# Kernel tuning notes

Measured on AMD Instinct MI355X. Metric: run time of the kernel, lower is better.

The kernel has to match this reference:

```python
import jax, jax.numpy as jnp
import numpy as np

N_NODES = 50000
NEG_SLOPE = 0.2  # PyG GATConv default
EPS = 1e-16      # PyG softmax denominator epsilon


def _gat_conv(x, edge_index, W, att_src, att_dst, bias):
    """Single-head PyG-style GATConv with self-loops.
    x: [N, F_in], edge_index: [2, E] (row 0 = src/j, row 1 = dst/i).
    """
    n = x.shape[0]
    loop = jnp.arange(n, dtype=edge_index.dtype)
    src = jnp.concatenate([edge_index[0], loop])  # [E+N]
    dst = jnp.concatenate([edge_index[1], loop])  # [E+N]

    h = x @ W                                      # [N, F_out]
    a_src = h @ att_src                            # [N]
    a_dst = h @ att_dst                            # [N]

    e = jax.nn.leaky_relu(a_src[src] + a_dst[dst], NEG_SLOPE)  # [E+N]
    # segment softmax over incoming edges of each dst node
    m = jax.ops.segment_max(e, dst, num_segments=n)
    m = jnp.where(jnp.isfinite(m), m, 0.0)
    e = jnp.exp(e - m[dst])
    s = jax.ops.segment_sum(e, dst, num_segments=n)
    alpha = e / (s[dst] + EPS)                     # [E+N]

    out = jax.ops.segment_sum(alpha[:, None] * h[src], dst, num_segments=n)
    return out + bias


def setup_inputs() -> dict:
    key = jax.random.key(0)
    ks = jax.random.split(key, 10)
    d_in, d_hid, d_emb = 128, 64, 64
    n_edges = 800000
    x = jax.random.normal(ks[0], (N_NODES, d_in), dtype=jnp.float32)
    edge_index = jax.random.randint(ks[1], (2, n_edges), 0, N_NODES, dtype=jnp.int64)
    def glorot(k, shape):
        lim = float(np.sqrt(6.0 / sum(shape)))
        return jax.random.uniform(k, shape, jnp.float32, -lim, lim)
    return {
        "x": x,
        "edge_index": edge_index,
        "W1": glorot(ks[2], (d_in, d_hid)),
        "att_src1": glorot(ks[3], (d_hid,)),
        "att_dst1": glorot(ks[4], (d_hid,)),
        "b1": jnp.zeros((d_hid,), jnp.float32),
        "W2": glorot(ks[5], (d_hid, d_emb)),
        "att_src2": glorot(ks[6], (d_emb,)),
        "att_dst2": glorot(ks[7], (d_emb,)),
        "b2": jnp.zeros((d_emb,), jnp.float32),
    }


def reference(x, edge_index, W1, att_src1, att_dst1, b1, W2, att_src2, att_dst2, b2):
    x1 = jax.nn.relu(_gat_conv(x, edge_index, W1, att_src1, att_dst1, b1))
    # dropout is identity in eval mode
    x2 = _gat_conv(x1, edge_index, W2, att_src2, att_dst2, b2)
    return x2
```

## Files before the change

kernel.cpp:

```cpp
#include <hip/hip_runtime.h>
#include <hip/hip_bf16.h>

#define F_OUT 64
#define NEG_SLOPE 0.2f
#define SOFT_EPS 1e-16f
#define BW 256
#define CH 8192
#define TH 512

typedef short short8 __attribute__((ext_vector_type(8)));
typedef float floatx4 __attribute__((ext_vector_type(4)));
typedef unsigned short ushort4v __attribute__((ext_vector_type(4)));

__device__ __forceinline__ unsigned short f2bf_bits(float v) {
    __hip_bfloat16 hb = __float2bfloat16(v);
    return *(unsigned short*)&hb;
}
__device__ __forceinline__ float bf_bits2f(unsigned short u) {
    __hip_bfloat16 hb = *(__hip_bfloat16*)&u;
    return __bfloat162float(hb);
}
__device__ __forceinline__ float read_any(const void* src, int off, int bf) {
    return bf ? __bfloat162float(((const __hip_bfloat16*)src)[off])
              : ((const float*)src)[off];
}
__device__ __forceinline__ int get_idx(const void* ei, int i64, long long pos) {
    return i64 ? (int)((const long long*)ei)[pos] : ((const int*)ei)[pos];
}

__device__ __forceinline__ void detect_local(const unsigned* wbits, const unsigned* ebits,
                                             int* sm_bf, int* sm_i64) {
    if (threadIdx.x < 64) {
        unsigned w = wbits[threadIdx.x];
        unsigned e = (w >> 7) & 0xFFu;
        unsigned long long mb = __ballot(e >= 0x60u && e <= 0x7Eu);
        unsigned long long mz = __ballot(ebits[2 * threadIdx.x + 1] == 0u);
        if (threadIdx.x == 0) { *sm_bf = (__popcll(mb) > 32); *sm_i64 = (__popcll(mz) > 32); }
    }
    __syncthreads();
}

__global__ void count_prep(const void* __restrict__ ei, int* __restrict__ table,
                           const void* w1, const void* as1, const void* ad1, const void* b1,
                           const void* w2, const void* as2, const void* ad2, const void* b2,
                           unsigned short* __restrict__ wt1, unsigned short* __restrict__ wt2,
                           float* __restrict__ vecs, int* __restrict__ flags,
                           int E, int total, int NB, int nchunks, int n1, int n2, int K1) {
    __shared__ int cnt[1024];
    __shared__ int s_bf, s_i64;
    detect_local((const unsigned*)w1, (const unsigned*)ei, &s_bf, &s_i64);
    int bf = s_bf, i64 = s_i64;
    int g = blockIdx.x, tid = threadIdx.x;
    if (g == 0 && tid == 0) { flags[0] = bf; flags[1] = i64; }

    if (g < nchunks) {
        for (int k = tid; k < NB; k += TH) cnt[k] = 0;
        __syncthreads();
        int base = g * CH;
        int lim = base + CH < total ? base + CH : total;
        for (int t = base + tid; t < lim; t += TH) {
            int i = t < E ? get_idx(ei, i64, (long long)E + t) : t - E;
            atomicAdd(&cnt[i >> 8], 1);
        }
        __syncthreads();
        for (int k = tid; k < NB; k += TH) table[k * nchunks + g] = cnt[k];
    } else {
        int wtotal = n1 + n2 + 384;
        for (int t = tid; t < wtotal; t += TH) {
            if (t < n1) {
                int n = t / K1, k = t - n * K1;
                wt1[t] = f2bf_bits(read_any(w1, k * F_OUT + n, bf));
            } else if (t < n1 + n2) {
                int u = t - n1;
                int n = u >> 6, k = u & 63;
                wt2[u] = f2bf_bits(read_any(w2, k * F_OUT + n, bf));
            } else {
                int u = t - n1 - n2;
                const void* srcp[6] = {as1, ad1, b1, as2, ad2, b2};
                vecs[u] = read_any(srcp[u >> 6], u & 63, bf);
            }
        }
    }
}

template <int K, int WAVES>
__device__ __forceinline__ void gemm_body(int blk, int tid,
                          const void* __restrict__ xv, const unsigned short* __restrict__ Wt,
                          const float* __restrict__ att_s, const float* __restrict__ att_d,
                          unsigned short* __restrict__ h, float* __restrict__ a_s,
                          float* __restrict__ a_d, int N, int bf) {
    int lane = tid & 63;
    int m0 = (blk * WAVES + (tid >> 6)) * 16;
    if (m0 >= N) return;
    int c = lane & 15, quad = lane >> 4;
    int arow = m0 + c;
    if (arow >= N) arow = N - 1;

    floatx4 acc0 = {0.f, 0.f, 0.f, 0.f};
    floatx4 acc1 = acc0, acc2 = acc0, acc3 = acc0;

    for (int kc = 0; kc < K; kc += 32) {
        int ka = kc + quad * 8;
        short8 a;
        if (bf) {
            a = *(const short8*)((const unsigned short*)xv + (size_t)arow * K + ka);
        } else {
            const float* xp = (const float*)xv + (size_t)arow * K + ka;
#pragma unroll
            for (int j = 0; j < 8; ++j) a[j] = (short)f2bf_bits(xp[j]);
        }
        short8 b0 = *(const short8*)(Wt + (size_t)(c)      * K + ka);
        short8 b1 = *(const short8*)(Wt + (size_t)(16 + c) * K + ka);
        short8 b2 = *(const short8*)(Wt + (size_t)(32 + c) * K + ka);
        short8 b3 = *(const short8*)(Wt + (size_t)(48 + c) * K + ka);
        acc0 = __builtin_amdgcn_mfma_f32_16x16x32_bf16(a, b0, acc0, 0, 0, 0);
        acc1 = __builtin_amdgcn_mfma_f32_16x16x32_bf16(a, b1, acc1, 0, 0, 0);
        acc2 = __builtin_amdgcn_mfma_f32_16x16x32_bf16(a, b2, acc2, 0, 0, 0);
        acc3 = __builtin_amdgcn_mfma_f32_16x16x32_bf16(a, b3, acc3, 0, 0, 0);
    }

    float as0 = att_s[c],      as1 = att_s[16 + c], as2 = att_s[32 + c], as3 = att_s[48 + c];
    float ad0 = att_d[c],      ad1 = att_d[16 + c], ad2 = att_d[32 + c], ad3 = att_d[48 + c];
#pragma unroll
    for (int reg = 0; reg < 4; ++reg) {
        int row = m0 + quad * 4 + reg;
        float vs = acc0[reg] * as0 + acc1[reg] * as1 + acc2[reg] * as2 + acc3[reg] * as3;
        float vd = acc0[reg] * ad0 + acc1[reg] * ad1 + acc2[reg] * ad2 + acc3[reg] * ad3;
#pragma unroll
        for (int off = 1; off < 16; off <<= 1) {
            vs += __shfl_xor(vs, off);
            vd += __shfl_xor(vd, off);
        }
        if (row < N) {
            if (c == 0) { a_s[row] = vs; a_d[row] = vd; }
            unsigned short* hr = h + (size_t)row * F_OUT + c;
            hr[0]  = f2bf_bits(acc0[reg]);
            hr[16] = f2bf_bits(acc1[reg]);
            hr[32] = f2bf_bits(acc2[reg]);
            hr[48] = f2bf_bits(acc3[reg]);
        }
    }
}

__global__ void __launch_bounds__(TH)
scatter_gemm1(const void* __restrict__ ei, const int* __restrict__ table,
              unsigned* __restrict__ staged, int* __restrict__ segbeg,
              int* __restrict__ row_ptr, const void* __restrict__ xv,
              const unsigned short* __restrict__ Wt,
              const float* __restrict__ att_s, const float* __restrict__ att_d,
              unsigned short* __restrict__ h, float* __restrict__ a_s,
              float* __restrict__ a_d, const unsigned* __restrict__ wbits,
              int E, int total, int NB, int nchunks, int N) {
    __shared__ int s_bf, s_i64;
    detect_local(wbits, (const unsigned*)ei, &s_bf, &s_i64);
    int tid = threadIdx.x;
    if ((int)blockIdx.x >= nchunks) {
        gemm_body<128, 8>(blockIdx.x - nchunks, tid, xv, Wt, att_s, att_d,
                          h, a_s, a_d, N, s_bf);
        return;
    }
    __shared__ int s_scan[TH];
    __shared__ int s_cur[1024];
    int g = blockIdx.x;
    int i64 = s_i64;
    int b0 = 0;
    if (tid < NB) {
        const int* row = table + (size_t)tid * nchunks;
        int rsum = 0, rpart = 0;
        for (int c2 = 0; c2 < nchunks; ++c2) {
            int v = row[c2];
            rsum += v;
            rpart += (c2 < g) ? v : 0;
        }
        b0 = rsum;
        s_cur[tid] = rpart;
    }
    s_scan[tid] = (tid < NB) ? b0 : 0;
    __syncthreads();
    for (int off = 1; off < TH; off <<= 1) {
        int v = (tid >= off) ? s_scan[tid - off] : 0;
        __syncthreads();
        s_scan[tid] += v;
        __syncthreads();
    }
    if (tid < NB) {
        int excl = s_scan[tid] - b0;
        s_cur[tid] = excl + s_cur[tid];
        if (g == 0) segbeg[tid] = excl;
    }
    if (g == 0 && tid == 0) { segbeg[NB] = total; row_ptr[N] = total; }
    __syncthreads();
    int base = g * CH;
    int lim = base + CH < total ? base + CH : total;
    for (int t = base + tid; t < lim; t += TH) {
        int i = t < E ? get_idx(ei, i64, (long long)E + t) : t - E;
        int j = t < E ? get_idx(ei, i64, t) : t - E;
        int pos = atomicAdd(&s_cur[i >> 8], 1);
        staged[pos] = ((unsigned)(i & 255) << 24) | (unsigned)j;
    }
}

__global__ void bucket_csr(const unsigned* __restrict__ staged, const int* __restrict__ segbeg,
                           int* __restrict__ row_ptr, int* __restrict__ eidx, int N) {
    __shared__ int ldeg[BW];
    __shared__ int lcur[BW];
    __shared__ int wtot[4];
    int b = blockIdx.x;
    int t = threadIdx.x;
    int seg_beg = segbeg[b];
    int seg_end = segbeg[b + 1];
    ldeg[t] = 0;
    __syncthreads();
    for (int p = seg_beg + t; p < seg_end; p += 256)
        atomicAdd(&ldeg[staged[p] >> 24], 1);
    __syncthreads();
    int lane = t & 63, w = t >> 6;
    int d = ldeg[t];
    int v = d;
#pragma unroll
    for (int off = 1; off < 64; off <<= 1) {
        int u = __shfl_up(v, off);
        if (lane >= off) v += u;
    }
    if (lane == 63) wtot[w] = v;
    __syncthreads();
    int woff = 0;
    for (int k = 0; k < w; ++k) woff += wtot[k];
    int excl = v - d + woff;
    int node = b * BW + t;
    if (node < N) row_ptr[node] = seg_beg + excl;
    lcur[t] = excl;
    __syncthreads();
    for (int p = seg_beg + t; p < seg_end; p += 256) {
        unsigned pk = staged[p];
        int pos = atomicAdd(&lcur[pk >> 24], 1);
        eidx[seg_beg + pos] = (int)(pk & 0xFFFFFFu);
    }
}

__global__ void mfma_gemm2(const void* __restrict__ xv, const unsigned short* __restrict__ Wt,
                           const float* __restrict__ att_s, const float* __restrict__ att_d,
                           unsigned short* __restrict__ h, float* __restrict__ a_s,
                           float* __restrict__ a_d, int N) {
    gemm_body<64, 4>(blockIdx.x, threadIdx.x, xv, Wt, att_s, att_d, h, a_s, a_d, N, 1);
}

__global__ void node_gather(const int* __restrict__ row_ptr, const int* __restrict__ eidx,
                            const float* __restrict__ a_s, const float* __restrict__ a_d,
                            const unsigned short* __restrict__ h, const float* __restrict__ bias,
                            void* __restrict__ out, int N,
                            const int* __restrict__ flags, int mode) {
    int lane = threadIdx.x & 63;
    int i = blockIdx.x * 4 + (threadIdx.x >> 6);
    if (i >= N) return;
    int quad = lane >> 4, c = lane & 15;
    int beg = row_ptr[i];
    int end = row_ptr[i + 1];
    float ad = a_d[i];
    float se = 0.f;
    floatx4 acc[4];
#pragma unroll
    for (int k = 0; k < 4; ++k) acc[k] = (floatx4){0.f, 0.f, 0.f, 0.f};

    for (int p = beg; p < end; p += 64) {
        int tile = end - p; if (tile > 64) tile = 64;
        int jm = eidx[p + (lane < tile ? lane : tile - 1)];
        float wm = 0.f;
        if (lane < tile) {
            float e = a_s[jm] + ad;
            wm = __expf(e > 0.f ? e : NEG_SLOPE * e);
        }
        se += wm;
        for (int e = 0; e < tile; e += 16) {
#pragma unroll
            for (int k = 0; k < 4; ++k) {
                if (e + 4 * k < tile) {
                    int idx = e + 4 * k + quad;
                    int srcl = idx < tile ? idx : tile - 1;
                    int jk = __shfl(jm, srcl);
                    float wk = __shfl(wm, srcl);
                    if (idx >= tile) wk = 0.f;
                    ushort4v hv = *(const ushort4v*)(h + (size_t)jk * F_OUT + (c << 2));
                    acc[k][0] += wk * bf_bits2f(hv[0]);
                    acc[k][1] += wk * bf_bits2f(hv[1]);
                    acc[k][2] += wk * bf_bits2f(hv[2]);
                    acc[k][3] += wk * bf_bits2f(hv[3]);
                }
            }
        }
    }
#pragma unroll
    for (int off = 1; off < 64; off <<= 1) se += __shfl_xor(se, off);
    floatx4 A = (acc[0] + acc[1]) + (acc[2] + acc[3]);
#pragma unroll
    for (int m = 0; m < 4; ++m) {
        A[m] += __shfl_xor(A[m], 16);
        A[m] += __shfl_xor(A[m], 32);
    }
    if (quad == 0) {
        int col = c << 2;
        float inv = 1.f / (se + SOFT_EPS);
        float v0 = A[0] * inv + bias[col];
        float v1 = A[1] * inv + bias[col + 1];
        float v2 = A[2] * inv + bias[col + 2];
        float v3 = A[3] * inv + bias[col + 3];
        size_t o = (size_t)i * F_OUT + col;
        if (mode == 0) {
            ushort4v ov;
            ov[0] = f2bf_bits(v0 > 0.f ? v0 : 0.f);
            ov[1] = f2bf_bits(v1 > 0.f ? v1 : 0.f);
            ov[2] = f2bf_bits(v2 > 0.f ? v2 : 0.f);
            ov[3] = f2bf_bits(v3 > 0.f ? v3 : 0.f);
            *(ushort4v*)((unsigned short*)out + o) = ov;
        } else if (flags[0]) {
            ushort4v ov;
            ov[0] = f2bf_bits(v0); ov[1] = f2bf_bits(v1);
            ov[2] = f2bf_bits(v2); ov[3] = f2bf_bits(v3);
            *(ushort4v*)((unsigned short*)out + o) = ov;
        } else {
            floatx4 ov = {v0, v1, v2, v3};
            *(floatx4*)((float*)out + o) = ov;
        }
    }
}

extern "C" void kernel_launch(void* const* d_in, const int* in_sizes, int n_in,
                              void* d_out, int out_size, void* d_ws, size_t ws_size,
                              hipStream_t stream) {
    const void* x   = d_in[0];
    const void* ei  = d_in[1];
    const void* W1  = d_in[2];
    const void* as1 = d_in[3];
    const void* ad1 = d_in[4];
    const void* b1  = d_in[5];
    const void* W2  = d_in[6];
    const void* as2 = d_in[7];
    const void* ad2 = d_in[8];
    const void* b2  = d_in[9];

    int E  = in_sizes[1] / 2;
    int n1 = in_sizes[2];
    int n2 = in_sizes[6];
    int K1 = n1 / F_OUT;
    int N  = in_sizes[0] / K1;
    int total = E + N;
    int NB = (N + BW - 1) / BW;
    int nchunks = (total + CH - 1) / CH;
    int M = NB * nchunks;

    size_t nf = (size_t)N * F_OUT;
    char* wsb = (char*)d_ws;
    unsigned short* h   = (unsigned short*)wsb;
    unsigned short* x1b = h + nf;
    unsigned short* wt1 = x1b + nf;
    unsigned short* wt2 = wt1 + n1;
    float* a_s  = (float*)(wt2 + n2 + ((n1 + n2) & 1));
    float* a_d  = a_s + N;
    float* vecs = a_d + N;
    float* cAs1 = vecs,       *cAd1 = vecs + 64,  *cB1 = vecs + 128;
    float* cAs2 = vecs + 192, *cAd2 = vecs + 256, *cB2 = vecs + 320;
    int* flags    = (int*)(vecs + 384);
    int* row_ptr  = flags + 8;
    int* eidx     = row_ptr + N + 1;
    unsigned* staged = (unsigned*)(eidx + total);
    int* table    = (int*)(staged + total);
    int* segbeg   = table + M;

    int blkG1 = (N + 127) / 128;
    int blkG2 = (N + 63) / 64;
    int blkNode = (N + 3) / 4;

    count_prep<<<nchunks + 1, TH, 0, stream>>>(ei, table, W1, as1, ad1, b1,
                                               W2, as2, ad2, b2, wt1, wt2, vecs, flags,
                                               E, total, NB, nchunks, n1, n2, K1);
    scatter_gemm1<<<nchunks + blkG1, TH, 0, stream>>>(ei, table, staged, segbeg, row_ptr,
                                                      x, wt1, cAs1, cAd1, h, a_s, a_d,
                                                      (const unsigned*)W1,
                                                      E, total, NB, nchunks, N);
    bucket_csr<<<NB, 256, 0, stream>>>(staged, segbeg, row_ptr, eidx, N);
    node_gather<<<blkNode, 256, 0, stream>>>(row_ptr, eidx, a_s, a_d, h, cB1, x1b, N, flags, 0);
    mfma_gemm2<<<blkG2, 256, 0, stream>>>(x1b, wt2, cAs2, cAd2, h, a_s, a_d, N);
    node_gather<<<blkNode, 256, 0, stream>>>(row_ptr, eidx, a_s, a_d, h, cB2, d_out, N, flags, 1);
}
```

Before: 207.1 us.

## Fuse layer-1 gather with layer-2 GEMM in one kernel

```diff
diff --git a/kernel.cpp b/kernel.cpp
--- a/kernel.cpp
+++ b/kernel.cpp
@@ -238,22 +238,13 @@
     }
 }
 
-__global__ void mfma_gemm2(const void* __restrict__ xv, const unsigned short* __restrict__ Wt,
-                           const float* __restrict__ att_s, const float* __restrict__ att_d,
-                           unsigned short* __restrict__ h, float* __restrict__ a_s,
-                           float* __restrict__ a_d, int N) {
-    gemm_body<64, 4>(blockIdx.x, threadIdx.x, xv, Wt, att_s, att_d, h, a_s, a_d, N, 1);
-}
-
-__global__ void node_gather(const int* __restrict__ row_ptr, const int* __restrict__ eidx,
-                            const float* __restrict__ a_s, const float* __restrict__ a_d,
-                            const unsigned short* __restrict__ h, const float* __restrict__ bias,
-                            void* __restrict__ out, int N,
-                            const int* __restrict__ flags, int mode) {
-    int lane = threadIdx.x & 63;
-    int i = blockIdx.x * 4 + (threadIdx.x >> 6);
-    if (i >= N) return;
-    int quad = lane >> 4, c = lane & 15;
+__device__ __forceinline__ void gather_node(int i, int lane, int quad, int c,
+                                            const int* __restrict__ row_ptr,
+                                            const int* __restrict__ eidx,
+                                            const float* __restrict__ a_s,
+                                            const float* __restrict__ a_d,
+                                            const unsigned short* __restrict__ h,
+                                            float* se_out, floatx4* A_out) {
     int beg = row_ptr[i];
     int end = row_ptr[i + 1];
     float ad = a_d[i];
@@ -297,6 +288,99 @@
         A[m] += __shfl_xor(A[m], 16);
         A[m] += __shfl_xor(A[m], 32);
     }
+    *se_out = se;
+    *A_out = A;
+}
+
+#define XST 72
+__global__ void __launch_bounds__(1024)
+gather1_gemm2(const int* __restrict__ row_ptr, const int* __restrict__ eidx,
+              const float* __restrict__ a_s, const float* __restrict__ a_d,
+              const unsigned short* __restrict__ h, const float* __restrict__ bias,
+              const unsigned short* __restrict__ Wt2,
+              const float* __restrict__ att_s2, const float* __restrict__ att_d2,
+              unsigned short* __restrict__ h2, float* __restrict__ a_s2,
+              float* __restrict__ a_d2, int N) {
+    __shared__ unsigned short x1t[16 * XST];
+    int tid = threadIdx.x;
+    int lane = tid & 63;
+    int wv = tid >> 6;
+    int quad = lane >> 4, c = lane & 15;
+    int i = blockIdx.x * 16 + wv;
+
+    if (i < N) {
+        float se; floatx4 A;
+        gather_node(i, lane, quad, c, row_ptr, eidx, a_s, a_d, h, &se, &A);
+        if (quad == 0) {
+            int col = c << 2;
+            float inv = 1.f / (se + SOFT_EPS);
+            float v0 = A[0] * inv + bias[col];
+            float v1 = A[1] * inv + bias[col + 1];
+            float v2 = A[2] * inv + bias[col + 2];
+            float v3 = A[3] * inv + bias[col + 3];
+            ushort4v ov;
+            ov[0] = f2bf_bits(v0 > 0.f ? v0 : 0.f);
+            ov[1] = f2bf_bits(v1 > 0.f ? v1 : 0.f);
+            ov[2] = f2bf_bits(v2 > 0.f ? v2 : 0.f);
+            ov[3] = f2bf_bits(v3 > 0.f ? v3 : 0.f);
+            *(ushort4v*)(x1t + wv * XST + col) = ov;
+        }
+    } else if (quad == 0) {
+        *(ushort4v*)(x1t + wv * XST + (c << 2)) = (ushort4v){0, 0, 0, 0};
+    }
+    __syncthreads();
+
+    if (wv == 0) {
+        int m0 = blockIdx.x * 16;
+        floatx4 acc0 = {0.f, 0.f, 0.f, 0.f};
+        floatx4 acc1 = acc0, acc2 = acc0, acc3 = acc0;
+#pragma unroll
+        for (int kc = 0; kc < 64; kc += 32) {
+            int ka = kc + quad * 8;
+            short8 a = *(const short8*)(x1t + c * XST + ka);
+            short8 b0 = *(const short8*)(Wt2 + (size_t)(c)      * 64 + ka);
+            short8 b1 = *(const short8*)(Wt2 + (size_t)(16 + c) * 64 + ka);
+            short8 b2 = *(const short8*)(Wt2 + (size_t)(32 + c) * 64 + ka);
+            short8 b3 = *(const short8*)(Wt2 + (size_t)(48 + c) * 64 + ka);
+            acc0 = __builtin_amdgcn_mfma_f32_16x16x32_bf16(a, b0, acc0, 0, 0, 0);
+            acc1 = __builtin_amdgcn_mfma_f32_16x16x32_bf16(a, b1, acc1, 0, 0, 0);
+            acc2 = __builtin_amdgcn_mfma_f32_16x16x32_bf16(a, b2, acc2, 0, 0, 0);
+            acc3 = __builtin_amdgcn_mfma_f32_16x16x32_bf16(a, b3, acc3, 0, 0, 0);
+        }
+        float as0 = att_s2[c],      as1 = att_s2[16 + c], as2 = att_s2[32 + c], as3 = att_s2[48 + c];
+        float ad0 = att_d2[c],      ad1 = att_d2[16 + c], ad2 = att_d2[32 + c], ad3 = att_d2[48 + c];
+#pragma unroll
+        for (int reg = 0; reg < 4; ++reg) {
+            int row = m0 + quad * 4 + reg;
+            float vs = acc0[reg] * as0 + acc1[reg] * as1 + acc2[reg] * as2 + acc3[reg] * as3;
+            float vd = acc0[reg] * ad0 + acc1[reg] * ad1 + acc2[reg] * ad2 + acc3[reg] * ad3;
+#pragma unroll
+            for (int off = 1; off < 16; off <<= 1) {
+                vs += __shfl_xor(vs, off);
+                vd += __shfl_xor(vd, off);
+            }
+            if (row < N) {
+                if (c == 0) { a_s2[row] = vs; a_d2[row] = vd; }
+                unsigned short* hr = h2 + (size_t)row * F_OUT + c;
+                hr[0]  = f2bf_bits(acc0[reg]);
+                hr[16] = f2bf_bits(acc1[reg]);
+                hr[32] = f2bf_bits(acc2[reg]);
+                hr[48] = f2bf_bits(acc3[reg]);
+            }
+        }
+    }
+}
+
+__global__ void node_gather_out(const int* __restrict__ row_ptr, const int* __restrict__ eidx,
+                                const float* __restrict__ a_s, const float* __restrict__ a_d,
+                                const unsigned short* __restrict__ h, const float* __restrict__ bias,
+                                void* __restrict__ out, int N, const int* __restrict__ flags) {
+    int lane = threadIdx.x & 63;
+    int i = blockIdx.x * 4 + (threadIdx.x >> 6);
+    if (i >= N) return;
+    int quad = lane >> 4, c = lane & 15;
+    float se; floatx4 A;
+    gather_node(i, lane, quad, c, row_ptr, eidx, a_s, a_d, h, &se, &A);
     if (quad == 0) {
         int col = c << 2;
         float inv = 1.f / (se + SOFT_EPS);
@@ -305,14 +389,7 @@
         float v2 = A[2] * inv + bias[col + 2];
         float v3 = A[3] * inv + bias[col + 3];
         size_t o = (size_t)i * F_OUT + col;
-        if (mode == 0) {
-            ushort4v ov;
-            ov[0] = f2bf_bits(v0 > 0.f ? v0 : 0.f);
-            ov[1] = f2bf_bits(v1 > 0.f ? v1 : 0.f);
-            ov[2] = f2bf_bits(v2 > 0.f ? v2 : 0.f);
-            ov[3] = f2bf_bits(v3 > 0.f ? v3 : 0.f);
-            *(ushort4v*)((unsigned short*)out + o) = ov;
-        } else if (flags[0]) {
+        if (flags[0]) {
             ushort4v ov;
             ov[0] = f2bf_bits(v0); ov[1] = f2bf_bits(v1);
             ov[2] = f2bf_bits(v2); ov[3] = f2bf_bits(v3);
@@ -351,12 +428,14 @@
     size_t nf = (size_t)N * F_OUT;
     char* wsb = (char*)d_ws;
     unsigned short* h   = (unsigned short*)wsb;
-    unsigned short* x1b = h + nf;
-    unsigned short* wt1 = x1b + nf;
+    unsigned short* h2  = h + nf;
+    unsigned short* wt1 = h2 + nf;
     unsigned short* wt2 = wt1 + n1;
     float* a_s  = (float*)(wt2 + n2 + ((n1 + n2) & 1));
     float* a_d  = a_s + N;
-    float* vecs = a_d + N;
+    float* a_s2 = a_d + N;
+    float* a_d2 = a_s2 + N;
+    float* vecs = a_d2 + N;
     float* cAs1 = vecs,       *cAd1 = vecs + 64,  *cB1 = vecs + 128;
     float* cAs2 = vecs + 192, *cAd2 = vecs + 256, *cB2 = vecs + 320;
     int* flags    = (int*)(vecs + 384);
@@ -367,7 +446,7 @@
     int* segbeg   = table + M;
 
     int blkG1 = (N + 127) / 128;
-    int blkG2 = (N + 63) / 64;
+    int blkFuse = (N + 15) / 16;
     int blkNode = (N + 3) / 4;
 
     count_prep<<<nchunks + 1, TH, 0, stream>>>(ei, table, W1, as1, ad1, b1,
@@ -378,7 +457,8 @@
                                                       (const unsigned*)W1,
                                                       E, total, NB, nchunks, N);
     bucket_csr<<<NB, 256, 0, stream>>>(staged, segbeg, row_ptr, eidx, N);
-    node_gather<<<blkNode, 256, 0, stream>>>(row_ptr, eidx, a_s, a_d, h, cB1, x1b, N, flags, 0);
-    mfma_gemm2<<<blkG2, 256, 0, stream>>>(x1b, wt2, cAs2, cAd2, h, a_s, a_d, N);
-    node_gather<<<blkNode, 256, 0, stream>>>(row_ptr, eidx, a_s, a_d, h, cB2, d_out, N, flags, 1);
-}
+    gather1_gemm2<<<blkFuse, 1024, 0, stream>>>(row_ptr, eidx, a_s, a_d, h, cB1,
+                                                wt2, cAs2, cAd2, h2, a_s2, a_d2, N);
+    node_gather_out<<<blkNode, 256, 0, stream>>>(row_ptr, eidx, a_s2, a_d2, h2, cB2,
+                                                 d_out, N, flags);
+}
```

Measured after the change: 206.5 us. Within noise of the previous version (-0.3%).
